# Kernel optimization log

Hardware: AMD Instinct MI355X
Metric: run time of the kernel (lower is better)

## Reference

```python
import jax, jax.numpy as jnp
import numpy as np
import math

D_MODEL = 1024
NUM_HEADS = 16
D_FF = 4096
LN_EPS = 1e-5


def _layer_norm(x, gamma, beta):
    mu = jnp.mean(x, axis=-1, keepdims=True)
    var = jnp.mean(jnp.square(x - mu), axis=-1, keepdims=True)
    return (x - mu) / jnp.sqrt(var + LN_EPS) * gamma + beta


def setup_inputs() -> dict:
    key = jax.random.key(0)
    ks = jax.random.split(key, 16)
    S, B, D, F = 2048, 2, D_MODEL, D_FF
    sc = 0.02
    inp = {
        "x": jax.random.normal(ks[0], (S, B, D), dtype=jnp.float32),
        "Wq": jax.random.normal(ks[1], (D, D), dtype=jnp.float32) * sc,
        "bq": jnp.zeros((D,), jnp.float32),
        "Wk": jax.random.normal(ks[2], (D, D), dtype=jnp.float32) * sc,
        "bk": jnp.zeros((D,), jnp.float32),
        "Wv": jax.random.normal(ks[3], (D, D), dtype=jnp.float32) * sc,
        "bv": jnp.zeros((D,), jnp.float32),
        "Wo": jax.random.normal(ks[4], (D, D), dtype=jnp.float32) * sc,
        "bo": jnp.zeros((D,), jnp.float32),
        "g1": jnp.ones((D,), jnp.float32),
        "b1": jnp.zeros((D,), jnp.float32),
        "W1": jax.random.normal(ks[5], (D, F), dtype=jnp.float32) * sc,
        "bb1": jnp.zeros((F,), jnp.float32),
        "W2": jax.random.normal(ks[6], (F, D), dtype=jnp.float32) * sc,
        "bb2": jnp.zeros((D,), jnp.float32),
        "g2": jnp.ones((D,), jnp.float32),
        "b2": jnp.zeros((D,), jnp.float32),
    }
    return inp


def reference(x, Wq, bq, Wk, bk, Wv, bv, Wo, bo, g1, b1, W1, bb1, W2, bb2, g2, b2):
    # x: [S, B, D] (seq-first, matching the torch module)
    S, B, D = x.shape
    H = NUM_HEADS
    dh = D // H

    def split_(t):  # [S, B, D] -> [B*H, S, dh]  (same as view + transpose in torch)
        return jnp.swapaxes(t.reshape(S, B * H, dh), 0, 1)

    q = split_(x @ Wq + bq)
    k = split_(x @ Wk + bk)
    v = split_(x @ Wv + bv)

    # naive bmm -> softmax -> bmm attention (full [B*H, S, S] scores)
    scores = jnp.einsum("nsd,ntd->nst", q / math.sqrt(dh), k)
    attn = jax.nn.softmax(scores, axis=-1)
    o = jnp.einsum("nst,ntd->nsd", attn, v)  # [B*H, S, dh]
    o = jnp.swapaxes(o, 0, 1).reshape(S, B, D) @ Wo + bo

    x1 = _layer_norm(x + o, g1, b1)
    ff = jax.nn.relu(x1 @ W1 + bb1) @ W2 + bb2
    return _layer_norm(x1 + ff, g2, b2)
```

## Files before the change

kernel.cpp:

```cpp
#include <hip/hip_runtime.h>
#include <hip/hip_bf16.h>
#include <cstdint>

typedef __bf16 bf16_t;
typedef __attribute__((ext_vector_type(8))) __bf16 bf16x8;
typedef __attribute__((ext_vector_type(4))) __bf16 bf16x4;
typedef __attribute__((ext_vector_type(2))) __bf16 bf16x2;
typedef __attribute__((ext_vector_type(4))) float f32x4;

#define GLOBAL_AS __attribute__((address_space(1)))
#define LDS_AS __attribute__((address_space(3)))

__device__ __forceinline__ void lds_load16(void* lds, const void* g) {
    __builtin_amdgcn_global_load_lds((GLOBAL_AS void*)g, (LDS_AS void*)lds, 16, 0, 0);
}

__global__ __launch_bounds__(256) void prep_all(const float* __restrict__ x,
                                                const float* __restrict__ Wq,
                                                const float* __restrict__ Wk,
                                                const float* __restrict__ Wv,
                                                const float* __restrict__ Wo,
                                                const float* __restrict__ W1,
                                                const float* __restrict__ W2,
                                                const float* __restrict__ bq,
                                                const float* __restrict__ bk,
                                                const float* __restrict__ bv,
                                                bf16_t* __restrict__ xb,
                                                bf16_t* __restrict__ WqkvT,
                                                bf16_t* __restrict__ WoT,
                                                bf16_t* __restrict__ W1T,
                                                bf16_t* __restrict__ W2T,
                                                float* __restrict__ qkvb) {
    __shared__ float T[64][65];
    const int bid = blockIdx.x, tid = threadIdx.x;
    if (bid < 3072) {
        const float* W; bf16_t* WT; int Kd, Nd, lb;
        if (bid < 1024) {
            Kd = 1024; Nd = 1024; lb = bid & 255;
            const int w = bid >> 8;
            W  = (w == 0) ? Wq : (w == 1) ? Wk : (w == 2) ? Wv : Wo;
            WT = (w == 0) ? WqkvT : (w == 1) ? WqkvT + 1048576
               : (w == 2) ? WqkvT + 2097152 : WoT;
        } else if (bid < 2048) { W = W1; WT = W1T; Kd = 1024; Nd = 4096; lb = bid - 1024; }
        else                   { W = W2; WT = W2T; Kd = 4096; Nd = 1024; lb = bid - 2048; }
        const int nbk = Kd >> 6;
        const int bk = lb % nbk, bn = lb / nbk;
        const int k0 = bk << 6, n0 = bn << 6;
        #pragma unroll
        for (int rep = 0; rep < 4; ++rep) {
            int r = rep * 16 + (tid >> 4);
            int c = (tid & 15) * 4;
            float4 v = *(const float4*)(W + (size_t)(k0 + r) * Nd + n0 + c);
            T[r][c] = v.x; T[r][c + 1] = v.y; T[r][c + 2] = v.z; T[r][c + 3] = v.w;
        }
        __syncthreads();
        #pragma unroll
        for (int rep = 0; rep < 4; ++rep) {
            int r = rep * 16 + (tid >> 4);
            int c = (tid & 15) * 4;
            bf16x4 o;
            o[0] = (bf16_t)T[c][r]; o[1] = (bf16_t)T[c + 1][r];
            o[2] = (bf16_t)T[c + 2][r]; o[3] = (bf16_t)T[c + 3][r];
            *(bf16x4*)(WT + (size_t)(n0 + r) * Kd + k0 + c) = o;
        }
    } else if (bid < 7168) {
        const int i = (bid - 3072) * 256 + tid;
        float4 v = *(const float4*)(x + (size_t)i * 4);
        bf16x4 o;
        o[0] = (bf16_t)v.x; o[1] = (bf16_t)v.y; o[2] = (bf16_t)v.z; o[3] = (bf16_t)v.w;
        *(bf16x4*)(xb + (size_t)i * 4) = o;
    } else {
        const int i = (bid - 7168) * 256 + tid;
        if (i < 3072)
            qkvb[i] = (i < 1024) ? bq[i] : (i < 2048) ? bk[i - 1024] : bv[i - 2048];
    }
}

template <int OM, bool RELU>
__global__ __launch_bounds__(512, 2) void gemm256(const bf16_t* __restrict__ A,
                                                  const bf16_t* __restrict__ Bt,
                                                  const float* __restrict__ bias,
                                                  void* __restrict__ Cv,
                                                  int M, int N, int K,
                                                  int kc_len, int n_kc) {
    __shared__ alignas(16) bf16_t As[2][256 * 64];
    __shared__ alignas(16) bf16_t Bs[2][256 * 64];
    const int tid = threadIdx.x;
    const int wid = tid >> 6, lane = tid & 63;
    const int lr = lane & 15, lg = lane >> 4;
    const int wr = wid >> 2, wc = wid & 3;
    const int lrsw = (lr & 7) << 4;

    const int nbn = N >> 8;
    const int nbase = (M >> 8) * nbn;
    const int nwg = nbase * n_kc;
    int bid = blockIdx.x;
    int wg;
    if ((nwg & 7) == 0) { int q = nwg >> 3; wg = (bid & 7) * q + (bid >> 3); }
    else wg = bid;
    const int kc = wg / nbase;
    const int inner = wg - kc * nbase;
    const int bm = inner / nbn, bn = inner % nbn;

    f32x4 acc[8][4];
    #pragma unroll
    for (int i = 0; i < 8; ++i)
        #pragma unroll
        for (int j = 0; j < 4; ++j) acc[i][j] = f32x4{0.f, 0.f, 0.f, 0.f};

    const int srow = wid * 16 + (lane >> 3);
    const int colbyte = (((lane & 7) ^ (lane >> 3)) << 4);
    const char* gA = (const char*)(A + ((size_t)(bm * 256 + srow) * K + kc * kc_len)) + colbyte;
    const char* gB = (const char*)(Bt + ((size_t)(bn * 256 + srow) * K + kc * kc_len)) + colbyte;
    const size_t rs8 = (size_t)8 * K * 2;
    const size_t rs128 = (size_t)128 * K * 2;

    auto stA = [&](int b, int half, int kt) {
        char* d = (char*)As[b] + (half * 128 + wid * 16) * 128;
        const char* s = gA + (size_t)half * rs128 + (size_t)kt * 128;
        lds_load16(d, s);
        lds_load16(d + 1024, s + rs8);
    };
    auto stB = [&](int b, int half, int kt) {
        char* d = (char*)Bs[b] + (half * 128 + wid * 16) * 128;
        const char* s = gB + (size_t)half * rs128 + (size_t)kt * 128;
        lds_load16(d, s);
        lds_load16(d + 1024, s + rs8);
    };
    auto ldA = [&](int b, int m, int kk) {
        const int row = (m >> 2) * 128 + (m & 3) * 32 + wr * 16 + lr;
        return *(const bf16x8*)((const char*)As[b] + row * 128 + ((kk * 64 + lg * 16) ^ lrsw));
    };
    auto ldB = [&](int b, int n, int kk) {
        const int row = n * 64 + wc * 16 + lr;
        return *(const bf16x8*)((const char*)Bs[b] + row * 128 + ((kk * 64 + lg * 16) ^ lrsw));
    };

    const int NT = kc_len >> 6;
    stA(0, 0, 0); stB(0, 0, 0); stB(0, 1, 0); stA(0, 1, 0);
    asm volatile("s_waitcnt vmcnt(4)" ::: "memory");
    __builtin_amdgcn_s_barrier();

    bf16x8 afr[4][2], bfr[4][2];
    #pragma unroll 1
    for (int kt = 0; kt < NT; ++kt) {
        const int buf = kt & 1;
        const int ktn = (kt + 1 < NT) ? kt + 1 : kt;

        #pragma unroll
        for (int m = 0; m < 4; ++m) {
            afr[m][0] = ldA(buf, m, 0);
            afr[m][1] = ldA(buf, m, 1);
        }
        #pragma unroll
        for (int n = 0; n < 2; ++n) {
            bfr[n][0] = ldB(buf, n, 0);
            bfr[n][1] = ldB(buf, n, 1);
        }
        stA(buf ^ 1, 0, ktn);
        __builtin_amdgcn_s_barrier();
        __builtin_amdgcn_s_setprio(1);
        #pragma unroll
        for (int m = 0; m < 4; ++m)
            #pragma unroll
            for (int n = 0; n < 2; ++n) {
                acc[m][n] = __builtin_amdgcn_mfma_f32_16x16x32_bf16(afr[m][0], bfr[n][0], acc[m][n], 0, 0, 0);
                acc[m][n] = __builtin_amdgcn_mfma_f32_16x16x32_bf16(afr[m][1], bfr[n][1], acc[m][n], 0, 0, 0);
            }
        __builtin_amdgcn_s_setprio(0);
        asm volatile("s_waitcnt vmcnt(4)" ::: "memory");
        __builtin_amdgcn_s_barrier();

        #pragma unroll
        for (int n = 2; n < 4; ++n) {
            bfr[n][0] = ldB(buf, n, 0);
            bfr[n][1] = ldB(buf, n, 1);
        }
        stB(buf ^ 1, 0, ktn);
        __builtin_amdgcn_s_barrier();
        __builtin_amdgcn_s_setprio(1);
        #pragma unroll
        for (int m = 0; m < 4; ++m)
            #pragma unroll
            for (int n = 2; n < 4; ++n) {
                acc[m][n] = __builtin_amdgcn_mfma_f32_16x16x32_bf16(afr[m][0], bfr[n][0], acc[m][n], 0, 0, 0);
                acc[m][n] = __builtin_amdgcn_mfma_f32_16x16x32_bf16(afr[m][1], bfr[n][1], acc[m][n], 0, 0, 0);
            }
        __builtin_amdgcn_s_setprio(0);
        asm volatile("s_waitcnt vmcnt(4)" ::: "memory");
        __builtin_amdgcn_s_barrier();

        #pragma unroll
        for (int m = 0; m < 4; ++m) {
            afr[m][0] = ldA(buf, m + 4, 0);
            afr[m][1] = ldA(buf, m + 4, 1);
        }
        stB(buf ^ 1, 1, ktn);
        __builtin_amdgcn_s_barrier();
        __builtin_amdgcn_s_setprio(1);
        #pragma unroll
        for (int m = 0; m < 4; ++m)
            #pragma unroll
            for (int n = 0; n < 2; ++n) {
                acc[m + 4][n] = __builtin_amdgcn_mfma_f32_16x16x32_bf16(afr[m][0], bfr[n][0], acc[m + 4][n], 0, 0, 0);
                acc[m + 4][n] = __builtin_amdgcn_mfma_f32_16x16x32_bf16(afr[m][1], bfr[n][1], acc[m + 4][n], 0, 0, 0);
            }
        __builtin_amdgcn_s_setprio(0);
        __builtin_amdgcn_s_barrier();

        stA(buf ^ 1, 1, ktn);
        __builtin_amdgcn_s_barrier();
        __builtin_amdgcn_s_setprio(1);
        #pragma unroll
        for (int m = 0; m < 4; ++m)
            #pragma unroll
            for (int n = 2; n < 4; ++n) {
                acc[m + 4][n] = __builtin_amdgcn_mfma_f32_16x16x32_bf16(afr[m][0], bfr[n][0], acc[m + 4][n], 0, 0, 0);
                acc[m + 4][n] = __builtin_amdgcn_mfma_f32_16x16x32_bf16(afr[m][1], bfr[n][1], acc[m + 4][n], 0, 0, 0);
            }
        __builtin_amdgcn_s_setprio(0);
        asm volatile("s_waitcnt vmcnt(4)" ::: "memory");
        __builtin_amdgcn_s_barrier();
    }

    float* outf = (float*)Cv + (size_t)kc * M * N;
    bf16_t* outb = (bf16_t*)Cv + (size_t)kc * M * N;
    float bv[4];
    #pragma unroll
    for (int n = 0; n < 4; ++n) {
        const int c = (bn << 8) + n * 64 + wc * 16 + lr;
        bv[n] = (bias && kc == 0) ? bias[c] : 0.f;
    }
    #pragma unroll
    for (int m = 0; m < 8; ++m) {
        const int row0 = (bm << 8) + (m >> 2) * 128 + (m & 3) * 32 + wr * 16 + (lg << 2);
        #pragma unroll
        for (int n = 0; n < 4; ++n) {
            const int c = (bn << 8) + n * 64 + wc * 16 + lr;
            #pragma unroll
            for (int j = 0; j < 4; ++j) {
                float v = acc[m][n][j] + bv[n];
                if (RELU) v = fmaxf(v, 0.f);
                if (OM == 0)      ((bf16_t*)Cv)[(size_t)(row0 + j) * N + c] = (bf16_t)v;
                else if (OM == 1) outf[(size_t)(row0 + j) * N + c] = v;
                else              outb[(size_t)(row0 + j) * N + c] = (bf16_t)v;
            }
        }
    }
}

__global__ __launch_bounds__(256) void reshape_v(const bf16_t* __restrict__ QKV,
                                                 bf16_t* __restrict__ VT) {
    __shared__ alignas(16) bf16_t Vl[64][72];
    const int n = blockIdx.x >> 5, st = blockIdx.x & 31;
    const int b = n >> 4, h = n & 15;
    const int s0 = st << 6;
    const int tid = threadIdx.x;

    #pragma unroll
    for (int rep = 0; rep < 2; ++rep) {
        int chunk = rep * 256 + tid;
        int sl = chunk >> 3, c8 = (chunk & 7) << 3;
        size_t srow = (size_t)(s0 + sl) * 2 + b;
        *(bf16x8*)&Vl[sl][c8] = *(const bf16x8*)(QKV + srow * 3072 + 2048 + h * 64 + c8);
    }
    __syncthreads();
    #pragma unroll
    for (int rep = 0; rep < 2; ++rep) {
        int chunk = rep * 256 + tid;
        int d = chunk >> 3, c8 = (chunk & 7) << 3;
        bf16x8 v;
        #pragma unroll
        for (int e = 0; e < 8; ++e) v[e] = Vl[c8 + e][d];
        *(bf16x8*)(VT + ((size_t)n * 64 + d) * 2048 + s0 + c8) = v;
    }
}

__global__ __launch_bounds__(256) void attn_fwd(const bf16_t* __restrict__ QKV,
                                                const bf16_t* __restrict__ VT,
                                                bf16_t* __restrict__ O) {
    const int S = 2048;
    const int n = blockIdx.x >> 4;
    const int qt = blockIdx.x & 15;
    const int q0 = qt << 7;
    const int b = n >> 4, h = n & 15;
    const int tid = threadIdx.x, wid = tid >> 6, lane = tid & 63;
    const int lr = lane & 15, lg = lane >> 4;
    const int lrsw = (lr & 7) << 4;

    __shared__ alignas(16) bf16_t Ks[2][64 * 64];
    __shared__ alignas(16) bf16_t Vs[2][64 * 64];
    __shared__ alignas(16) bf16_t Ps[4][2][16 * 64];

    char* pbs0 = (char*)&Ps[wid][0][0];
    char* pbs1 = (char*)&Ps[wid][1][0];

    const float qsc = 0.125f * 1.4426950408889634f;
    auto scale8 = [&](bf16x8 v) {
        bf16x8 r;
        #pragma unroll
        for (int e = 0; e < 8; ++e) r[e] = (bf16_t)((float)v[e] * qsc);
        return r;
    };
    const bf16_t* Qrow0 = QKV + ((size_t)(q0 + wid * 32 + lr) * 2 + b) * 3072 + h * 64;
    const bf16_t* Qrow1 = Qrow0 + (size_t)16 * 2 * 3072;
    const bf16x8 qa0 = scale8(*(const bf16x8*)(Qrow0 + lg * 8));
    const bf16x8 qa1 = scale8(*(const bf16x8*)(Qrow0 + 32 + lg * 8));
    const bf16x8 qb0 = scale8(*(const bf16x8*)(Qrow1 + lg * 8));
    const bf16x8 qb1 = scale8(*(const bf16x8*)(Qrow1 + 32 + lg * 8));

    bf16x8 ones;
    #pragma unroll
    for (int e = 0; e < 8; ++e) ones[e] = (bf16_t)1.0f;

    const int colbyte = (((lane & 7) ^ (lane >> 3)) << 4);
    const size_t kstride = (size_t)2 * 3072 * 2;
    const char* ksrc0 = (const char*)QKV +
        (((size_t)(wid * 16 + (lane >> 3)) * 2 + b) * 3072 + 1024 + h * 64) * 2 + colbyte;
    const char* ksrc1 = ksrc0 + 8 * kstride;
    const char* vsrc0 = (const char*)(VT + ((size_t)n * 64 + wid * 16 + (lane >> 3)) * S) + colbyte;
    const char* vsrc1 = vsrc0 + (size_t)8 * S * 2;

    auto stage = [&](int bf, int t0) {
        lds_load16((char*)Ks[bf] + wid * 2048,        ksrc0 + (size_t)t0 * kstride);
        lds_load16((char*)Ks[bf] + wid * 2048 + 1024, ksrc1 + (size_t)t0 * kstride);
        lds_load16((char*)Vs[bf] + wid * 2048,        vsrc0 + (size_t)t0 * 2);
        lds_load16((char*)Vs[bf] + wid * 2048 + 1024, vsrc1 + (size_t)t0 * 2);
    };

    f32x4 oaccA[4], oaccB[4];
    #pragma unroll
    for (int i = 0; i < 4; ++i) {
        oaccA[i] = f32x4{0.f, 0.f, 0.f, 0.f};
        oaccB[i] = f32x4{0.f, 0.f, 0.f, 0.f};
    }
    f32x4 laccA = f32x4{0.f, 0.f, 0.f, 0.f};
    f32x4 laccB = f32x4{0.f, 0.f, 0.f, 0.f};

    stage(0, 0);
    int buf = 0;

    #pragma unroll 1
    for (int t0 = 0; t0 < S; t0 += 64) {
        if (t0 + 64 < S) {
            stage(buf ^ 1, t0 + 64);
            asm volatile("s_waitcnt vmcnt(4)" ::: "memory");
        } else {
            asm volatile("s_waitcnt vmcnt(0)" ::: "memory");
        }
        __builtin_amdgcn_s_barrier();

        const char* kb = (char*)Ks[buf];
        const char* vb = (char*)Vs[buf];

        f32x4 swA[4], swB[4];
        __builtin_amdgcn_s_setprio(1);
        #pragma unroll
        for (int tc = 0; tc < 4; ++tc) {
            const char* krow = kb + (tc * 16 + lr) * 128;
            bf16x8 kf0 = *(const bf16x8*)(krow + ((lg * 16) ^ lrsw));
            bf16x8 kf1 = *(const bf16x8*)(krow + ((64 + lg * 16) ^ lrsw));
            f32x4 za = f32x4{-12.f, -12.f, -12.f, -12.f};
            za = __builtin_amdgcn_mfma_f32_16x16x32_bf16(kf0, qa0, za, 0, 0, 0);
            za = __builtin_amdgcn_mfma_f32_16x16x32_bf16(kf1, qa1, za, 0, 0, 0);
            swA[tc] = za;
            f32x4 zb = f32x4{-12.f, -12.f, -12.f, -12.f};
            zb = __builtin_amdgcn_mfma_f32_16x16x32_bf16(kf0, qb0, zb, 0, 0, 0);
            zb = __builtin_amdgcn_mfma_f32_16x16x32_bf16(kf1, qb1, zb, 0, 0, 0);
            swB[tc] = zb;
        }
        __builtin_amdgcn_s_setprio(0);

        #pragma unroll
        for (int tc = 0; tc < 4; ++tc)
            #pragma unroll
            for (int j = 0; j < 4; ++j) {
                swA[tc][j] = __builtin_amdgcn_exp2f(swA[tc][j]);
                swB[tc][j] = __builtin_amdgcn_exp2f(swB[tc][j]);
            }

        #pragma unroll
        for (int tc = 0; tc < 4; ++tc) {
            bf16x4 pa, pb;
            pa[0] = (bf16_t)swA[tc][0]; pa[1] = (bf16_t)swA[tc][1];
            pa[2] = (bf16_t)swA[tc][2]; pa[3] = (bf16_t)swA[tc][3];
            pb[0] = (bf16_t)swB[tc][0]; pb[1] = (bf16_t)swB[tc][1];
            pb[2] = (bf16_t)swB[tc][2]; pb[3] = (bf16_t)swB[tc][3];
            const int off = (tc * 32 + lg * 8) ^ lrsw;
            *(bf16x4*)(pbs0 + lr * 128 + off) = pa;
            *(bf16x4*)(pbs1 + lr * 128 + off) = pb;
        }
        bf16x8 pA0 = *(const bf16x8*)(pbs0 + lr * 128 + ((lg * 16) ^ lrsw));
        bf16x8 pA1 = *(const bf16x8*)(pbs0 + lr * 128 + ((64 + lg * 16) ^ lrsw));
        bf16x8 pB0 = *(const bf16x8*)(pbs1 + lr * 128 + ((lg * 16) ^ lrsw));
        bf16x8 pB1 = *(const bf16x8*)(pbs1 + lr * 128 + ((64 + lg * 16) ^ lrsw));

        __builtin_amdgcn_s_setprio(1);
        laccA = __builtin_amdgcn_mfma_f32_16x16x32_bf16(ones, pA0, laccA, 0, 0, 0);
        laccA = __builtin_amdgcn_mfma_f32_16x16x32_bf16(ones, pA1, laccA, 0, 0, 0);
        laccB = __builtin_amdgcn_mfma_f32_16x16x32_bf16(ones, pB0, laccB, 0, 0, 0);
        laccB = __builtin_amdgcn_mfma_f32_16x16x32_bf16(ones, pB1, laccB, 0, 0, 0);

        #pragma unroll
        for (int vc = 0; vc < 4; ++vc) {
            const char* vrow = vb + (vc * 16 + lr) * 128;
            bf16x8 vf0 = *(const bf16x8*)(vrow + ((lg * 16) ^ lrsw));
            bf16x8 vf1 = *(const bf16x8*)(vrow + ((64 + lg * 16) ^ lrsw));
            oaccA[vc] = __builtin_amdgcn_mfma_f32_16x16x32_bf16(vf0, pA0, oaccA[vc], 0, 0, 0);
            oaccA[vc] = __builtin_amdgcn_mfma_f32_16x16x32_bf16(vf1, pA1, oaccA[vc], 0, 0, 0);
            oaccB[vc] = __builtin_amdgcn_mfma_f32_16x16x32_bf16(vf0, pB0, oaccB[vc], 0, 0, 0);
            oaccB[vc] = __builtin_amdgcn_mfma_f32_16x16x32_bf16(vf1, pB1, oaccB[vc], 0, 0, 0);
        }
        __builtin_amdgcn_s_setprio(0);
        __builtin_amdgcn_s_barrier();
        buf ^= 1;
    }

    const float invA = 1.0f / laccA[0];
    const float invB = 1.0f / laccB[0];
    const size_t tokA = (size_t)(q0 + wid * 32 + lr) * 2 + b;
    const size_t tokB = tokA + 32;
    #pragma unroll
    for (int vc = 0; vc < 4; ++vc) {
        bf16x4 oa, ob;
        #pragma unroll
        for (int j = 0; j < 4; ++j) {
            oa[j] = (bf16_t)(oaccA[vc][j] * invA);
            ob[j] = (bf16_t)(oaccB[vc][j] * invB);
        }
        *(bf16x4*)(O + tokA * 1024 + h * 64 + vc * 16 + lg * 4) = oa;
        *(bf16x4*)(O + tokB * 1024 + h * 64 + vc * 16 + lg * 4) = ob;
    }
}

template <int P>
__global__ __launch_bounds__(256) void ln_res(const bf16_t* __restrict__ X,
                                              const bf16_t* __restrict__ Y,
                                              const float* __restrict__ g,
                                              const float* __restrict__ be,
                                              float* __restrict__ outf,
                                              bf16_t* __restrict__ outb) {
    const int row = blockIdx.x, tid = threadIdx.x;
    const size_t base = (size_t)row * 1024 + tid * 4;
    const size_t pstride = (size_t)4096 * 1024;
    bf16x4 xv = *(const bf16x4*)(X + base);
    float v0 = (float)xv[0], v1 = (float)xv[1], v2 = (float)xv[2], v3 = (float)xv[3];
    #pragma unroll
    for (int p = 0; p < P; ++p) {
        bf16x4 yv = *(const bf16x4*)(Y + p * pstride + base);
        v0 += (float)yv[0]; v1 += (float)yv[1]; v2 += (float)yv[2]; v3 += (float)yv[3];
    }
    float s = v0 + v1 + v2 + v3;
    float sq = v0 * v0 + v1 * v1 + v2 * v2 + v3 * v3;
    #pragma unroll
    for (int m = 1; m < 64; m <<= 1) {
        s += __shfl_xor(s, m);
        sq += __shfl_xor(sq, m);
    }
    __shared__ float rs[4], rq[4];
    const int wid = tid >> 6;
    if ((tid & 63) == 0) { rs[wid] = s; rq[wid] = sq; }
    __syncthreads();
    s = rs[0] + rs[1] + rs[2] + rs[3];
    sq = rq[0] + rq[1] + rq[2] + rq[3];
    const float mu = s * (1.f / 1024.f);
    const float var = sq * (1.f / 1024.f) - mu * mu;
    const float rstd = rsqrtf(var + 1e-5f);
    float4 gv = *(const float4*)(g + tid * 4);
    float4 bv = *(const float4*)(be + tid * 4);
    float o0 = (v0 - mu) * rstd * gv.x + bv.x;
    float o1 = (v1 - mu) * rstd * gv.y + bv.y;
    float o2 = (v2 - mu) * rstd * gv.z + bv.z;
    float o3 = (v3 - mu) * rstd * gv.w + bv.w;
    if (outf) {
        float4 ov = {o0, o1, o2, o3};
        *(float4*)(outf + base) = ov;
    }
    if (outb) {
        bf16x4 ob;
        ob[0] = (bf16_t)o0; ob[1] = (bf16_t)o1; ob[2] = (bf16_t)o2; ob[3] = (bf16_t)o3;
        *(bf16x4*)(outb + base) = ob;
    }
}

extern "C" void kernel_launch(void* const* d_in, const int* in_sizes, int n_in,
                              void* d_out, int out_size, void* d_ws, size_t ws_size,
                              hipStream_t stream) {
    (void)in_sizes; (void)n_in; (void)out_size; (void)ws_size;
    const float* x   = (const float*)d_in[0];
    const float* Wq  = (const float*)d_in[1];
    const float* bq  = (const float*)d_in[2];
    const float* Wk  = (const float*)d_in[3];
    const float* bk  = (const float*)d_in[4];
    const float* Wv  = (const float*)d_in[5];
    const float* bv  = (const float*)d_in[6];
    const float* Wo  = (const float*)d_in[7];
    const float* bo  = (const float*)d_in[8];
    const float* g1  = (const float*)d_in[9];
    const float* b1  = (const float*)d_in[10];
    const float* W1  = (const float*)d_in[11];
    const float* bb1 = (const float*)d_in[12];
    const float* W2  = (const float*)d_in[13];
    const float* bb2 = (const float*)d_in[14];
    const float* g2  = (const float*)d_in[15];
    const float* b2  = (const float*)d_in[16];
    float* out = (float*)d_out;

    char* ws = (char*)d_ws;
    const size_t MB = 1ull << 20;
    bf16_t* xb    = (bf16_t*)(ws + 0);
    bf16_t* WqkvT = (bf16_t*)(ws + 8 * MB);
    bf16_t* WoT   = (bf16_t*)(ws + 14 * MB);
    bf16_t* W1T   = (bf16_t*)(ws + 16 * MB);
    bf16_t* W2T   = (bf16_t*)(ws + 24 * MB);
    float*  qkvb  = (float*)(ws + 32 * MB);
    bf16_t* QKV   = (bf16_t*)(ws + 33 * MB);
    bf16_t* VTh   = (bf16_t*)(ws + 57 * MB);
    bf16_t* Otok  = (bf16_t*)(ws + 65 * MB);
    bf16_t* WoP   = (bf16_t*)(ws + 73 * MB);
    bf16_t* x1b   = (bf16_t*)(ws + 105 * MB);
    bf16_t* Hff   = (bf16_t*)(ws + 113 * MB);
    bf16_t* W2P   = (bf16_t*)(ws + 33 * MB);

    prep_all<<<7180, 256, 0, stream>>>(x, Wq, Wk, Wv, Wo, W1, W2, bq, bk, bv,
                                       xb, WqkvT, WoT, W1T, W2T, qkvb);

    gemm256<0, false><<<192, 512, 0, stream>>>(xb, WqkvT, qkvb, QKV, 4096, 3072, 1024, 1024, 1);
    reshape_v<<<1024, 256, 0, stream>>>(QKV, VTh);
    attn_fwd<<<512, 256, 0, stream>>>(QKV, VTh, Otok);
    gemm256<2, false><<<256, 512, 0, stream>>>(Otok, WoT, bo, WoP, 4096, 1024, 1024, 256, 4);
    ln_res<4><<<4096, 256, 0, stream>>>(xb, WoP, g1, b1, nullptr, x1b);

    gemm256<0, true><<<256, 512, 0, stream>>>(x1b, W1T, bb1, Hff, 4096, 4096, 1024, 1024, 1);
    gemm256<2, false><<<256, 512, 0, stream>>>(Hff, W2T, bb2, W2P, 4096, 1024, 4096, 1024, 4);
    ln_res<4><<<4096, 256, 0, stream>>>(x1b, W2P, g2, b2, out, nullptr);
}
```

Measured before the change: 225.9 us.

## Split attention over the key dimension into two partial passes plus combine kernel

The attention kernel now splits the key/value sequence into two halves, doubling the grid from 512 to 1024 blocks so more of the GPU's compute units stay busy. Each block writes unnormalized fp32 partial outputs and row sums, and a new combine_o kernel adds the two halves, normalizes and writes bf16. This depends on the fixed softmax offset (no running max), which lets the partials be summed directly. The cost is an extra kernel launch and about 32MB of fp32 partial traffic, stored in the WoP workspace region.

```diff
diff --git a/kernel.cpp b/kernel.cpp
--- a/kernel.cpp
+++ b/kernel.cpp
@@ -278,10 +278,12 @@
 
 __global__ __launch_bounds__(256) void attn_fwd(const bf16_t* __restrict__ QKV,
                                                 const bf16_t* __restrict__ VT,
-                                                bf16_t* __restrict__ O) {
+                                                float* __restrict__ Opart,
+                                                float* __restrict__ lpart) {
     const int S = 2048;
-    const int n = blockIdx.x >> 4;
-    const int qt = blockIdx.x & 15;
+    const int n = blockIdx.x >> 5;
+    const int qt = (blockIdx.x >> 1) & 15;
+    const int sp = blockIdx.x & 1;
     const int q0 = qt << 7;
     const int b = n >> 4, h = n & 15;
     const int tid = threadIdx.x, wid = tid >> 6, lane = tid & 63;
@@ -314,11 +316,12 @@
     for (int e = 0; e < 8; ++e) ones[e] = (bf16_t)1.0f;
 
     const int colbyte = (((lane & 7) ^ (lane >> 3)) << 4);
+    const int tbase = sp << 10;
     const size_t kstride = (size_t)2 * 3072 * 2;
     const char* ksrc0 = (const char*)QKV +
-        (((size_t)(wid * 16 + (lane >> 3)) * 2 + b) * 3072 + 1024 + h * 64) * 2 + colbyte;
+        (((size_t)(tbase + wid * 16 + (lane >> 3)) * 2 + b) * 3072 + 1024 + h * 64) * 2 + colbyte;
     const char* ksrc1 = ksrc0 + 8 * kstride;
-    const char* vsrc0 = (const char*)(VT + ((size_t)n * 64 + wid * 16 + (lane >> 3)) * S) + colbyte;
+    const char* vsrc0 = (const char*)(VT + ((size_t)n * 64 + wid * 16 + (lane >> 3)) * S + tbase) + colbyte;
     const char* vsrc1 = vsrc0 + (size_t)8 * S * 2;
 
     auto stage = [&](int bf, int t0) {
@@ -341,8 +344,8 @@
     int buf = 0;
 
     #pragma unroll 1
-    for (int t0 = 0; t0 < S; t0 += 64) {
-        if (t0 + 64 < S) {
+    for (int t0 = 0; t0 < 1024; t0 += 64) {
+        if (t0 + 64 < 1024) {
             stage(buf ^ 1, t0 + 64);
             asm volatile("s_waitcnt vmcnt(4)" ::: "memory");
         } else {
@@ -416,21 +419,42 @@
         buf ^= 1;
     }
 
-    const float invA = 1.0f / laccA[0];
-    const float invB = 1.0f / laccB[0];
-    const size_t tokA = (size_t)(q0 + wid * 32 + lr) * 2 + b;
-    const size_t tokB = tokA + 32;
+    const int qrowA = q0 + wid * 32 + lr;
+    const int qrowB = qrowA + 16;
+    float* Op = Opart + (size_t)sp * 4096 * 1024;
+    const size_t tokA = (size_t)qrowA * 2 + b;
+    const size_t tokB = (size_t)qrowB * 2 + b;
     #pragma unroll
     for (int vc = 0; vc < 4; ++vc) {
-        bf16x4 oa, ob;
-        #pragma unroll
-        for (int j = 0; j < 4; ++j) {
-            oa[j] = (bf16_t)(oaccA[vc][j] * invA);
-            ob[j] = (bf16_t)(oaccB[vc][j] * invB);
-        }
-        *(bf16x4*)(O + tokA * 1024 + h * 64 + vc * 16 + lg * 4) = oa;
-        *(bf16x4*)(O + tokB * 1024 + h * 64 + vc * 16 + lg * 4) = ob;
-    }
+        f32x4 oa = oaccA[vc], ob = oaccB[vc];
+        *(f32x4*)(Op + tokA * 1024 + h * 64 + vc * 16 + lg * 4) = oa;
+        *(f32x4*)(Op + tokB * 1024 + h * 64 + vc * 16 + lg * 4) = ob;
+    }
+    if (lg == 0) {
+        lpart[(size_t)sp * 65536 + n * 2048 + qrowA] = laccA[0];
+        lpart[(size_t)sp * 65536 + n * 2048 + qrowB] = laccB[0];
+    }
+}
+
+__global__ __launch_bounds__(256) void combine_o(const float* __restrict__ Opart,
+                                                 const float* __restrict__ lpart,
+                                                 bf16_t* __restrict__ O) {
+    const int tok = blockIdx.x, tid = threadIdx.x;
+    const int c = tid * 4;
+    const int h = c >> 6;
+    const int q = tok >> 1, b = tok & 1;
+    const int n = b * 16 + h;
+    const float l = lpart[n * 2048 + q] + lpart[65536 + n * 2048 + q];
+    const float inv = 1.0f / l;
+    const size_t base = (size_t)tok * 1024 + c;
+    float4 a = *(const float4*)(Opart + base);
+    float4 d = *(const float4*)(Opart + (size_t)4096 * 1024 + base);
+    bf16x4 o;
+    o[0] = (bf16_t)((a.x + d.x) * inv);
+    o[1] = (bf16_t)((a.y + d.y) * inv);
+    o[2] = (bf16_t)((a.z + d.z) * inv);
+    o[3] = (bf16_t)((a.w + d.w) * inv);
+    *(bf16x4*)(O + base) = o;
 }
 
 template <int P>
@@ -514,9 +538,11 @@
     bf16_t* W1T   = (bf16_t*)(ws + 16 * MB);
     bf16_t* W2T   = (bf16_t*)(ws + 24 * MB);
     float*  qkvb  = (float*)(ws + 32 * MB);
+    float*  lpart = (float*)(ws + 32 * MB + 64 * 1024);
     bf16_t* QKV   = (bf16_t*)(ws + 33 * MB);
     bf16_t* VTh   = (bf16_t*)(ws + 57 * MB);
     bf16_t* Otok  = (bf16_t*)(ws + 65 * MB);
+    float*  Opart = (float*)(ws + 73 * MB);
     bf16_t* WoP   = (bf16_t*)(ws + 73 * MB);
     bf16_t* x1b   = (bf16_t*)(ws + 105 * MB);
     bf16_t* Hff   = (bf16_t*)(ws + 113 * MB);
@@ -527,7 +553,8 @@
 
     gemm256<0, false><<<192, 512, 0, stream>>>(xb, WqkvT, qkvb, QKV, 4096, 3072, 1024, 1024, 1);
     reshape_v<<<1024, 256, 0, stream>>>(QKV, VTh);
-    attn_fwd<<<512, 256, 0, stream>>>(QKV, VTh, Otok);
+    attn_fwd<<<1024, 256, 0, stream>>>(QKV, VTh, Opart, lpart);
+    combine_o<<<4096, 256, 0, stream>>>(Opart, lpart, Otok);
     gemm256<2, false><<<256, 512, 0, stream>>>(Otok, WoT, bo, WoP, 4096, 1024, 1024, 256, 4);
     ln_res<4><<<4096, 256, 0, stream>>>(xb, WoP, g1, b1, nullptr, x1b);
 
```

Result: slower. 235.5 us (+4.3%).
